# Kernel tuning notes

Hardware: AMD Instinct MI355X
Metric: run time of the kernel (lower is better)

## Reference

```python
import jax, jax.numpy as jnp
import numpy as np


def setup_inputs() -> dict:
    key = jax.random.key(0)
    k1, k2, k3 = jax.random.split(key, 3)
    x = jax.random.normal(k1, (32, 256, 32, 32), dtype=jnp.float32)
    weight = jax.random.normal(k2, (256, 256, 3, 3), dtype=jnp.float32) * 0.05
    bias = jax.random.normal(k3, (256,), dtype=jnp.float32) * 0.01
    return {"x": x, "weight": weight, "bias": bias}


def _forward(x, weight, bias):
    B, cin, n, _ = x.shape
    cout, _, k, _ = weight.shape
    s = (k - 1) // 2
    nf = n // 2 + 1
    bins = n * nf

    # fft shift matrix: exp(-1j*2*pi*s*(i+j)/n), kept rfft columns
    idx = jnp.arange(n)
    shift = idx[None, :] + idx[:, None]                     # (n, n)
    shift_m = jnp.exp(-1j * 2 * jnp.pi * s * shift / n)[:, :nf]
    shift_m = shift_m.reshape(bins, 1, 1).astype(jnp.complex64)

    # xfft: (B, cin, n, nf) -> (bins, cin, B)
    xfft = jnp.fft.rfft2(x)
    xfft = jnp.transpose(xfft, (2, 3, 1, 0)).reshape(bins, cin, B)

    # Hfft: (cout, cin, n, nf) -> (bins, cout, cin), shifted + conj
    Hfft = jnp.fft.rfft2(weight, s=(n, n)).reshape(cout, cin, bins)
    Hfft = shift_m * jnp.conj(jnp.transpose(Hfft, (2, 0, 1)))

    def sq_abs(z):
        return jnp.real(z) ** 2 + jnp.imag(z) ** 2

    RowNorm = jnp.sqrt(jnp.sum(sq_abs(Hfft), axis=2))       # (bins, cout)
    ColNorm = jnp.sqrt(jnp.sum(sq_abs(Hfft), axis=1))       # (bins, cin)

    if cout >= cin:
        RowLoss = jnp.mean((RowNorm - jnp.sqrt(cin / cout)) ** 2)
        ColLoss = jnp.mean((ColNorm - 1.0) ** 2)
        HHT = jnp.einsum('npc,nqc->npq', jnp.conj(Hfft), Hfft)  # (bins, cout, cout)
        mask = jnp.triu(jnp.ones((cout, cout), bool), k=1)
        count = bins * (cout * (cout - 1) // 2)
        AngLoss = jnp.sum(sq_abs(HHT) * mask[None]) / count   # MSE(|HHT[triu]|, 0)
        L = cout * ColLoss + cin * RowLoss + AngLoss
    else:
        RowLoss = jnp.mean((RowNorm - 1.0) ** 2)
        ColLoss = jnp.mean((ColNorm - jnp.sqrt(cout / cin)) ** 2)
        HTH = jnp.einsum('ndp,ndq->npq', jnp.conj(Hfft), Hfft)  # (bins, cin, cin)
        mask = jnp.triu(jnp.ones((cin, cin), bool), k=1)
        count = bins * (cin * (cin - 1) // 2)
        AngLoss = jnp.sum(sq_abs(HTH) * mask[None]) / count
        L = cout * ColLoss + cin * RowLoss + AngLoss

    # per-bin complex matmul: (bins, cout, cin) @ (bins, cin, B) -> (bins, cout, B)
    yfft = Hfft @ xfft
    yfft = jnp.transpose(yfft.reshape(n, nf, cout, B), (3, 2, 0, 1))  # (B, cout, n, nf)
    y = jnp.fft.irfft2(yfft, s=(n, n))
    y = y + bias[None, :, None, None]
    return y, L


def reference(x, weight, bias):
    return _forward(x, weight, bias)
```

## Files before the change

kernel.cpp:

```cpp
#include <hip/hip_runtime.h>
#include <math.h>

typedef __attribute__((ext_vector_type(8)))  short  short8;
typedef __attribute__((ext_vector_type(16))) float  float16;

#define TWO_PI_OVER_32 0.19634954084936207f

static __device__ __forceinline__ unsigned short f2bf(float f) {
    unsigned int u = __float_as_uint(f);
    u = (u + 0x7FFFu + ((u >> 16) & 1u)) >> 16;
    return (unsigned short)u;
}
static __device__ __forceinline__ float bf2f(unsigned short s) {
    return __uint_as_float(((unsigned int)s) << 16);
}

static __device__ __forceinline__ void g2l16(const void* g, void* l) {
    __builtin_amdgcn_global_load_lds(
        (const __attribute__((address_space(1))) unsigned int*)g,
        (__attribute__((address_space(3))) unsigned int*)l, 16, 0, 0);
}

#define SBAR() do { __builtin_amdgcn_s_barrier(); \
                    __builtin_amdgcn_sched_barrier(0); } while (0)
#define WAITV(n) do { asm volatile("s_waitcnt vmcnt(" #n ")" ::: "memory"); \
                      __builtin_amdgcn_sched_barrier(0); } while (0)

__global__ __launch_bounds__(256) void k_prepx(const float* __restrict__ x,
                                               unsigned short* __restrict__ xb,
                                               const float* __restrict__ w,
                                               unsigned short* __restrict__ wt,
                                               unsigned short* __restrict__ Vb,
                                               float* __restrict__ Drow,
                                               float* __restrict__ Dcol) {
    int tid = threadIdx.x;
    if (blockIdx.x < 4096) {
        int g = blockIdx.x * 256 + tid;
        int c = g & 31, r = (g >> 5) & 31, cig = (g >> 10) & 31, b = g >> 15;
        const float* xp = x + ((b * 256 + cig * 8) * 32 + r) * 32 + c;
        union { unsigned short u[8]; uint4 v; } pk;
        #pragma unroll
        for (int u = 0; u < 8; ++u) pk.u[u] = f2bf(xp[u * 1024]);
        ((uint4*)xb)[g] = pk.v;
        return;
    }
    __shared__ float sdata[45];
    __shared__ float ws2[256 * 9];
    int blk = blockIdx.x - 4096, lane = tid & 63;
    bool colmode = blk >= 256;
    int pc = blk & 255;
    if (tid < 45) sdata[tid] = 0.f;

    int p = colmode ? tid : pc;
    int c = colmode ? pc : tid;
    float w9[9];
    #pragma unroll
    for (int t = 0; t < 9; ++t) w9[t] = w[(p * 256 + c) * 9 + t];
    if (!colmode) {
        #pragma unroll
        for (int t = 0; t < 9; ++t) ws2[tid * 9 + t] = w9[t];
    }
    __syncthreads();

    int idx = 0;
    for (int ta = 0; ta < 9; ++ta)
        for (int tb = ta; tb < 9; ++tb) {
            float v = w9[ta] * w9[tb];
            #pragma unroll
            for (int off = 32; off > 0; off >>= 1) v += __shfl_down(v, off);
            if (lane == 0) atomicAdd(&sdata[idx], v);
            ++idx;
        }
    __syncthreads();
    if (tid < 45) (colmode ? Dcol : Drow)[tid * 256 + pc] = sdata[tid];

    if (!colmode) {
        #pragma unroll
        for (int t = 0; t < 9; ++t)
            wt[t * 65536 + (c >> 3) * 2048 + p * 8 + (c & 7)] = f2bf(w9[t]);
        if (tid < 320) {
            int ta = tid >> 5, cig = tid & 31;
            union { unsigned short u[8]; uint4 v; } pk;
            #pragma unroll
            for (int u = 0; u < 8; ++u)
                pk.u[u] = (ta < 9) ? f2bf(ws2[(cig * 8 + u) * 9 + ta]) : (unsigned short)0;
            ((uint4*)Vb)[(p * 10 + ta) * 32 + cig] = pk.v;
        }
    }
}

__global__ __launch_bounds__(256, 2) void k_conv(const unsigned short* __restrict__ xb,
                                                 const unsigned short* __restrict__ wt,
                                                 const float* __restrict__ bias,
                                                 const unsigned short* __restrict__ Vb,
                                                 unsigned short* __restrict__ Gb,
                                                 float* __restrict__ y) {
    __shared__ unsigned short xs[2][640 * 8];
    __shared__ unsigned short wsm[2][1152 * 8];

    const int tid  = threadIdx.x;
    const int lane = tid & 63;
    const int half = lane >> 5;
    const int m    = lane & 31;

    if (blockIdx.x >= 512) {
        int blk = blockIdx.x - 512, I = 0;
        while (blk >= 20 - I) { blk -= 20 - I; ++I; }
        int J = I + blk;
        const int wave = tid >> 6;
        const int wm = wave >> 1, wn = wave & 1;
        const int row0 = I * 128 + wm * 64;
        const int col0 = J * 128 + wn * 64;

        float16 acc[2][2];
        #pragma unroll
        for (int i = 0; i < 2; ++i)
            #pragma unroll
            for (int j = 0; j < 2; ++j)
                #pragma unroll
                for (int r = 0; r < 16; ++r) acc[i][j][r] = 0.f;

        const short8* vb = (const short8*)Vb;
        for (int kc = 0; kc < 16; ++kc) {
            int cig = kc * 2 + half;
            short8 a0 = vb[(row0 + m) * 32 + cig];
            short8 a1 = vb[(row0 + 32 + m) * 32 + cig];
            short8 b0 = vb[(col0 + m) * 32 + cig];
            short8 b1 = vb[(col0 + 32 + m) * 32 + cig];
            acc[0][0] = __builtin_amdgcn_mfma_f32_32x32x16_bf16(a0, b0, acc[0][0], 0, 0, 0);
            acc[0][1] = __builtin_amdgcn_mfma_f32_32x32x16_bf16(a0, b1, acc[0][1], 0, 0, 0);
            acc[1][0] = __builtin_amdgcn_mfma_f32_32x32x16_bf16(a1, b0, acc[1][0], 0, 0, 0);
            acc[1][1] = __builtin_amdgcn_mfma_f32_32x32x16_bf16(a1, b1, acc[1][1], 0, 0, 0);
        }
        #pragma unroll
        for (int i = 0; i < 2; ++i)
            #pragma unroll
            for (int j = 0; j < 2; ++j)
                #pragma unroll
                for (int reg = 0; reg < 16; ++reg) {
                    int crow = (reg & 3) + 8 * (reg >> 2) + 4 * half;
                    Gb[(row0 + i * 32 + crow) * 2560 + col0 + j * 32 + m] =
                        f2bf(acc[i][j][reg]);
                }
        return;
    }

    const int wv    = tid >> 6;
    const int id    = blockIdx.x;
    const int xcd   = id & 7;
    const int local = id >> 3;
    const int b     = xcd * 4 + (local >> 4);
    const int rem   = local & 15;
    const int co0   = (rem & 3) * 64;
    const int r0    = (rem >> 2) * 8;

    float16 acc[2][2];
    #pragma unroll
    for (int i = 0; i < 2; ++i)
        #pragma unroll
        for (int ns = 0; ns < 2; ++ns)
            #pragma unroll
            for (int r = 0; r < 16; ++r) acc[i][ns][r] = 0.f;

    const uint4* xbv = (const uint4*)xb;
    const uint4* wtv = (const uint4*)wt;

    const int cigl = lane >> 5;
    const int coll = lane & 31;

    auto stage = [&](int buf, int kc) {
        uint4* xd = (uint4*)xs[buf];
        uint4* wd = (uint4*)wsm[buf];
        #pragma unroll
        for (int ch = wv; ch < 28; ch += 4) {
            if (ch < 10) {
                int gr = (r0 + ch + 31) & 31;
                g2l16(&xbv[((b * 32 + kc * 2 + cigl) * 32 + gr) * 32 + coll],
                      &xd[ch * 64]);
            } else {
                int wc = ch - 10;
                int t = wc >> 1, cig = wc & 1;
                g2l16(&wtv[t * 8192 + (kc * 2 + cig) * 256 + co0 + lane],
                      &wd[wc * 64]);
            }
        }
    };

    auto compute = [&](int buf) {
        const short8* xsl = (const short8*)xs[buf];
        const short8* wsl = (const short8*)wsm[buf];
        #pragma unroll
        for (int btv = 0; btv < 3; ++btv) {
            short8 a0[3], a1[3];
            #pragma unroll
            for (int atv = 0; atv < 3; ++atv) {
                int t = atv * 3 + btv;
                a0[atv] = wsl[(t * 2 + half) * 64 + m];
                a1[atv] = wsl[(t * 2 + half) * 64 + 32 + m];
            }
            #pragma unroll
            for (int s = 0; s < 4; ++s) {
                short8 bf = xsl[((wv * 2 + s) * 2 + half) * 32 + ((m + btv + 31) & 31)];
                #pragma unroll
                for (int atv = 0; atv < 3; ++atv) {
                    int ns = s - atv;
                    if (ns >= 0 && ns < 2) {
                        acc[0][ns] = __builtin_amdgcn_mfma_f32_32x32x16_bf16(a0[atv], bf, acc[0][ns], 0, 0, 0);
                        acc[1][ns] = __builtin_amdgcn_mfma_f32_32x32x16_bf16(a1[atv], bf, acc[1][ns], 0, 0, 0);
                    }
                }
            }
        }
    };

    stage(0, 0);
    #pragma unroll 1
    for (int kc2 = 0; kc2 < 8; ++kc2) {
        stage(1, 2 * kc2 + 1);
        WAITV(7); SBAR();
        __builtin_amdgcn_s_setprio(1);
        compute(0);
        __builtin_amdgcn_s_setprio(0);
        SBAR();
        if (kc2 < 7) { stage(0, 2 * kc2 + 2); WAITV(7); }
        else         { WAITV(0); }
        SBAR();
        __builtin_amdgcn_s_setprio(1);
        compute(1);
        __builtin_amdgcn_s_setprio(0);
        if (kc2 < 7) SBAR();
    }

    #pragma unroll
    for (int i = 0; i < 2; ++i) {
        #pragma unroll
        for (int ns = 0; ns < 2; ++ns) {
            int r = r0 + wv * 2 + ns;
            #pragma unroll
            for (int reg = 0; reg < 16; ++reg) {
                int crow = (reg & 3) + 8 * (reg >> 2) + 4 * half;
                int co = co0 + i * 32 + crow;
                y[(b * 256 + co) * 1024 + r * 32 + m] = acc[i][ns][reg] + bias[co];
            }
        }
    }
}

__global__ __launch_bounds__(256) void k_loss(const float* __restrict__ Drow,
                                              const float* __restrict__ Dcol,
                                              const unsigned short* __restrict__ Gb,
                                              float* __restrict__ rowp,
                                              float* __restrict__ colp,
                                              float* __restrict__ angp) {
    __shared__ union {
        struct { float coef[45]; float red[2]; } rc;
        struct { unsigned short gs[9 * 2560]; float red; } ang;
    } sh;
    int tid = threadIdx.x;

    if (blockIdx.x < 544) {
        int bin = blockIdx.x;
        int u = bin / 17, v = bin % 17;
        if (tid < 2) sh.rc.red[tid] = 0.f;
        if (tid < 45) {
            int idx = 0, TA = 0, TB = 0;
            for (int ta = 0; ta < 9; ++ta)
                for (int tb = ta; tb < 9; ++tb) {
                    if (idx == tid) { TA = ta; TB = tb; }
                    ++idx;
                }
            int da = TA / 3 - TB / 3;
            int db = TA % 3 - TB % 3;
            float cth = cosf(TWO_PI_OVER_32 * (float)(u * da + v * db));
            sh.rc.coef[tid] = (TA == TB) ? 1.f : 2.f * cth;
        }
        __syncthreads();

        float s1 = 0.f, s2 = 0.f;
        const float* dr = Drow + tid;
        const float* dc = Dcol + tid;
        #pragma unroll
        for (int i = 0; i < 45; ++i) {
            s1 += sh.rc.coef[i] * dr[i * 256];
            s2 += sh.rc.coef[i] * dc[i * 256];
        }
        float e1 = sqrtf(fmaxf(s1, 0.f)) - 1.f; e1 *= e1;
        float e2 = sqrtf(fmaxf(s2, 0.f)) - 1.f; e2 *= e2;
        #pragma unroll
        for (int off = 32; off > 0; off >>= 1) {
            e1 += __shfl_down(e1, off);
            e2 += __shfl_down(e2, off);
        }
        if ((tid & 63) == 0) { atomicAdd(&sh.rc.red[0], e1); atomicAdd(&sh.rc.red[1], e2); }
        __syncthreads();
        if (tid == 0) { rowp[bin] = sh.rc.red[0]; colp[bin] = sh.rc.red[1]; }
    } else {
        int p = blockIdx.x - 544;
        if (tid == 0) sh.ang.red = 0.f;
        uint4* gsv = (uint4*)sh.ang.gs;
        const uint4* gbv = (const uint4*)Gb;
        for (int i = tid; i < 2880; i += 256) {
            int rr = i / 320, cc = i - rr * 320;
            gsv[i] = gbv[(p * 10 + rr) * 320 + cc];
        }
        __syncthreads();

        int q = tid;
        float S = 0.f;
        if (q > p) {
            float g5[5][5];
            #pragma unroll
            for (int i = 0; i < 5; ++i)
                #pragma unroll
                for (int j = 0; j < 5; ++j) g5[i][j] = 0.f;
            #pragma unroll
            for (int ta = 0; ta < 9; ++ta)
                #pragma unroll
                for (int tb = 0; tb < 9; ++tb) {
                    float c = bf2f(sh.ang.gs[ta * 2560 + q * 10 + tb]);
                    g5[ta / 3 - tb / 3 + 2][ta % 3 - tb % 3 + 2] += c;
                }
            #pragma unroll
            for (int da = 0; da < 5; ++da) {
                const float* g = g5[da];
                float sq = g[0]*g[0] + g[1]*g[1] + g[2]*g[2] + g[3]*g[3] + g[4]*g[4];
                float cr = g[0]*g[2] + g[1]*g[3] + g[2]*g[4] + g[0]*g[4];
                S += 17.f * sq + 2.f * cr;
            }
            S *= 32.f;
        }
        #pragma unroll
        for (int off = 32; off > 0; off >>= 1) S += __shfl_down(S, off);
        if ((tid & 63) == 0) atomicAdd(&sh.ang.red, S);
        __syncthreads();
        if (tid == 0) angp[p] = sh.ang.red;
    }
}

__global__ __launch_bounds__(256) void k_fin(const float* __restrict__ rowp,
                                             const float* __restrict__ colp,
                                             const float* __restrict__ angp,
                                             float* __restrict__ out) {
    __shared__ float sred[3][4];
    int tid = threadIdx.x;
    float r = 0.f, c = 0.f, a = 0.f;
    for (int i = tid; i < 544; i += 256) { r += rowp[i]; c += colp[i]; }
    a = angp[tid];
    #pragma unroll
    for (int off = 32; off > 0; off >>= 1) {
        r += __shfl_down(r, off);
        c += __shfl_down(c, off);
        a += __shfl_down(a, off);
    }
    if ((tid & 63) == 0) {
        int wv = tid >> 6;
        sred[0][wv] = r; sred[1][wv] = c; sred[2][wv] = a;
    }
    __syncthreads();
    if (tid == 0) {
        float R = sred[0][0] + sred[0][1] + sred[0][2] + sred[0][3];
        float C = sred[1][0] + sred[1][1] + sred[1][2] + sred[1][3];
        float A = sred[2][0] + sred[2][1] + sred[2][2] + sred[2][3];
        out[8388608] = R / 544.f + C / 544.f + A / (544.f * 32640.f);
    }
}

extern "C" void kernel_launch(void* const* d_in, const int* in_sizes, int n_in,
                              void* d_out, int out_size, void* d_ws, size_t ws_size,
                              hipStream_t stream) {
    const float* x    = (const float*)d_in[0];
    const float* w    = (const float*)d_in[1];
    const float* bias = (const float*)d_in[2];
    float* out = (float*)d_out;

    char* ws = (char*)d_ws;
    unsigned short* wt = (unsigned short*)ws;
    unsigned short* xb = (unsigned short*)(ws + 1179648);
    unsigned short* Vb = (unsigned short*)(ws + 17956864);
    float* Drow  = (float*)(ws + 19267584);
    float* Dcol  = (float*)(ws + 19313664);
    float* rowp  = (float*)(ws + 19359744);
    float* colp  = (float*)(ws + 19361920);
    float* angp  = (float*)(ws + 19364096);
    unsigned short* Gb = (unsigned short*)(ws + 19392512);

    k_prepx <<<4608, 256, 0, stream>>>(x, xb, w, wt, Vb, Drow, Dcol);
    k_conv  <<<722, 256, 0, stream>>>(xb, wt, bias, Vb, Gb, out);
    k_loss  <<<800, 256, 0, stream>>>(Drow, Dcol, Gb, rowp, colp, angp);
    k_fin   <<<1, 256, 0, stream>>>(rowp, colp, angp, out);
}
```

Baseline: 156.2 us.

## Load conv input tiles directly into registers instead of staging through LDS

```diff
diff --git a/kernel.cpp b/kernel.cpp
--- a/kernel.cpp
+++ b/kernel.cpp
@@ -95,7 +95,6 @@
                                                  const unsigned short* __restrict__ Vb,
                                                  unsigned short* __restrict__ Gb,
                                                  float* __restrict__ y) {
-    __shared__ unsigned short xs[2][640 * 8];
     __shared__ unsigned short wsm[2][1152 * 8];
 
     const int tid  = threadIdx.x;
@@ -162,32 +161,33 @@
             #pragma unroll
             for (int r = 0; r < 16; ++r) acc[i][ns][r] = 0.f;
 
-    const uint4* xbv = (const uint4*)xb;
-    const uint4* wtv = (const uint4*)wt;
-
-    const int cigl = lane >> 5;
-    const int coll = lane & 31;
-
-    auto stage = [&](int buf, int kc) {
-        uint4* xd = (uint4*)xs[buf];
+    const uint4*  wtv = (const uint4*)wt;
+    const short8* xg  = (const short8*)xb;
+
+    auto stage_w = [&](int buf, int kc) {
         uint4* wd = (uint4*)wsm[buf];
         #pragma unroll
-        for (int ch = wv; ch < 28; ch += 4) {
-            if (ch < 10) {
-                int gr = (r0 + ch + 31) & 31;
-                g2l16(&xbv[((b * 32 + kc * 2 + cigl) * 32 + gr) * 32 + coll],
-                      &xd[ch * 64]);
-            } else {
-                int wc = ch - 10;
-                int t = wc >> 1, cig = wc & 1;
-                g2l16(&wtv[t * 8192 + (kc * 2 + cig) * 256 + co0 + lane],
-                      &wd[wc * 64]);
-            }
+        for (int wc = wv; wc < 18; wc += 4) {
+            int t = wc >> 1, cig = wc & 1;
+            g2l16(&wtv[t * 8192 + (kc * 2 + cig) * 256 + co0 + lane],
+                  &wd[wc * 64]);
         }
     };
 
-    auto compute = [&](int buf) {
-        const short8* xsl = (const short8*)xs[buf];
+    auto load_x = [&](short8 (&xr)[12], int kc) {
+        #pragma unroll
+        for (int btv = 0; btv < 3; ++btv) {
+            int gc = (m + btv + 31) & 31;
+            #pragma unroll
+            for (int s = 0; s < 4; ++s) {
+                int gr = (r0 + wv * 2 + s + 31) & 31;
+                xr[btv * 4 + s] =
+                    xg[((b * 32 + kc * 2 + half) * 32 + gr) * 32 + gc];
+            }
+        }
+    };
+
+    auto compute = [&](int buf, const short8 (&xr)[12]) {
         const short8* wsl = (const short8*)wsm[buf];
         #pragma unroll
         for (int btv = 0; btv < 3; ++btv) {
@@ -200,7 +200,7 @@
             }
             #pragma unroll
             for (int s = 0; s < 4; ++s) {
-                short8 bf = xsl[((wv * 2 + s) * 2 + half) * 32 + ((m + btv + 31) & 31)];
+                short8 bf = xr[btv * 4 + s];
                 #pragma unroll
                 for (int atv = 0; atv < 3; ++atv) {
                     int ns = s - atv;
@@ -213,22 +213,37 @@
         }
     };
 
-    stage(0, 0);
+    short8 xA[12], xB[12];
+    stage_w(0, 0);
+    load_x(xA, 0);
     #pragma unroll 1
     for (int kc2 = 0; kc2 < 8; ++kc2) {
-        stage(1, 2 * kc2 + 1);
-        WAITV(7); SBAR();
-        __builtin_amdgcn_s_setprio(1);
-        compute(0);
-        __builtin_amdgcn_s_setprio(0);
-        SBAR();
-        if (kc2 < 7) { stage(0, 2 * kc2 + 2); WAITV(7); }
-        else         { WAITV(0); }
-        SBAR();
-        __builtin_amdgcn_s_setprio(1);
-        compute(1);
-        __builtin_amdgcn_s_setprio(0);
-        if (kc2 < 7) SBAR();
+        {
+            int kc = 2 * kc2;
+            stage_w(1, kc + 1);
+            load_x(xB, kc + 1);
+            if (wv < 2) { WAITV(17); } else { WAITV(16); }
+            SBAR();
+            __builtin_amdgcn_s_setprio(1);
+            compute(0, xA);
+            __builtin_amdgcn_s_setprio(0);
+            SBAR();
+        }
+        {
+            int kc = 2 * kc2 + 1;
+            if (kc2 < 7) {
+                stage_w(0, kc + 1);
+                load_x(xA, kc + 1);
+                if (wv < 2) { WAITV(17); } else { WAITV(16); }
+            } else {
+                WAITV(0);
+            }
+            SBAR();
+            __builtin_amdgcn_s_setprio(1);
+            compute(1, xB);
+            __builtin_amdgcn_s_setprio(0);
+            if (kc2 < 7) SBAR();
+        }
     }
 
     #pragma unroll
@@ -269,7 +284,7 @@
                     if (idx == tid) { TA = ta; TB = tb; }
                     ++idx;
                 }
-            int da = TA / 3 - TB / 3;
+        int da = TA / 3 - TB / 3;
             int db = TA % 3 - TB % 3;
             float cth = cosf(TWO_PI_OVER_32 * (float)(u * da + v * db));
             sh.rc.coef[tid] = (TA == TB) ? 1.f : 2.f * cth;
```

Measured after the change: 164.8 us. 5.5% more time.

## Single-buffer x tile in LDS to fit three blocks per CU, reorder block dispatch

Applied to the files above, without the earlier changes.

```diff
diff --git a/kernel.cpp b/kernel.cpp
--- a/kernel.cpp
+++ b/kernel.cpp
@@ -89,13 +89,13 @@
     }
 }
 
-__global__ __launch_bounds__(256, 2) void k_conv(const unsigned short* __restrict__ xb,
+__global__ __launch_bounds__(256, 3) void k_conv(const unsigned short* __restrict__ xb,
                                                  const unsigned short* __restrict__ wt,
                                                  const float* __restrict__ bias,
                                                  const unsigned short* __restrict__ Vb,
                                                  unsigned short* __restrict__ Gb,
                                                  float* __restrict__ y) {
-    __shared__ unsigned short xs[2][640 * 8];
+    __shared__ unsigned short xs[640 * 8];
     __shared__ unsigned short wsm[2][1152 * 8];
 
     const int tid  = threadIdx.x;
@@ -103,8 +103,8 @@
     const int half = lane >> 5;
     const int m    = lane & 31;
 
-    if (blockIdx.x >= 512) {
-        int blk = blockIdx.x - 512, I = 0;
+    if (blockIdx.x < 210) {
+        int blk = blockIdx.x, I = 0;
         while (blk >= 20 - I) { blk -= 20 - I; ++I; }
         int J = I + blk;
         const int wave = tid >> 6;
@@ -146,7 +146,7 @@
     }
 
     const int wv    = tid >> 6;
-    const int id    = blockIdx.x;
+    const int id    = blockIdx.x - 210;
     const int xcd   = id & 7;
     const int local = id >> 3;
     const int b     = xcd * 4 + (local >> 4);
@@ -168,26 +168,27 @@
     const int cigl = lane >> 5;
     const int coll = lane & 31;
 
-    auto stage = [&](int buf, int kc) {
-        uint4* xd = (uint4*)xs[buf];
+    auto stage_x = [&](int kc) {
+        uint4* xd = (uint4*)xs;
+        #pragma unroll
+        for (int ch = wv; ch < 10; ch += 4) {
+            int gr = (r0 + ch + 31) & 31;
+            g2l16(&xbv[((b * 32 + kc * 2 + cigl) * 32 + gr) * 32 + coll],
+                  &xd[ch * 64]);
+        }
+    };
+    auto stage_w = [&](int buf, int kc) {
         uint4* wd = (uint4*)wsm[buf];
         #pragma unroll
-        for (int ch = wv; ch < 28; ch += 4) {
-            if (ch < 10) {
-                int gr = (r0 + ch + 31) & 31;
-                g2l16(&xbv[((b * 32 + kc * 2 + cigl) * 32 + gr) * 32 + coll],
-                      &xd[ch * 64]);
-            } else {
-                int wc = ch - 10;
-                int t = wc >> 1, cig = wc & 1;
-                g2l16(&wtv[t * 8192 + (kc * 2 + cig) * 256 + co0 + lane],
-                      &wd[wc * 64]);
-            }
+        for (int wc = wv; wc < 18; wc += 4) {
+            int t = wc >> 1, cig = wc & 1;
+            g2l16(&wtv[t * 8192 + (kc * 2 + cig) * 256 + co0 + lane],
+                  &wd[wc * 64]);
         }
     };
 
     auto compute = [&](int buf) {
-        const short8* xsl = (const short8*)xs[buf];
+        const short8* xsl = (const short8*)xs;
         const short8* wsl = (const short8*)wsm[buf];
         #pragma unroll
         for (int btv = 0; btv < 3; ++btv) {
@@ -213,22 +214,23 @@
         }
     };
 
-    stage(0, 0);
+    stage_w(0, 0);
+    stage_x(0);
     #pragma unroll 1
-    for (int kc2 = 0; kc2 < 8; ++kc2) {
-        stage(1, 2 * kc2 + 1);
-        WAITV(7); SBAR();
+    for (int kc = 0; kc < 16; ++kc) {
+        int buf = kc & 1;
+        if (kc < 15) {
+            stage_w(buf ^ 1, kc + 1);
+            if (wv < 2) { WAITV(5); } else { WAITV(4); }
+        } else {
+            WAITV(0);
+        }
+        SBAR();
         __builtin_amdgcn_s_setprio(1);
-        compute(0);
+        compute(buf);
         __builtin_amdgcn_s_setprio(0);
         SBAR();
-        if (kc2 < 7) { stage(0, 2 * kc2 + 2); WAITV(7); }
-        else         { WAITV(0); }
-        SBAR();
-        __builtin_amdgcn_s_setprio(1);
-        compute(1);
-        __builtin_amdgcn_s_setprio(0);
-        if (kc2 < 7) SBAR();
+        if (kc < 15) stage_x(kc + 1);
     }
 
     #pragma unroll
```

Measured after the change: 154.6 us. About the same (-1.0%).
